# Kernel optimization log

Measured on AMD Instinct MI355X. Metric: run time of the kernel, lower is better.

The kernel has to match this reference:

```python
import jax, jax.numpy as jnp
import numpy as np

REG = 0.05  # reg_param > 0 -> entropic (logsumexp) branch
N, M, D = 16384, 8192, 128


def setup_inputs() -> dict:
    key = jax.random.key(0)
    k1, k2, k3 = jax.random.split(key, 3)
    source_data = jax.random.normal(k1, (N, D), dtype=jnp.float32)
    target_data = jax.random.normal(k2, (M, D), dtype=jnp.float32)
    psi = jax.random.normal(k3, (M,), dtype=jnp.float32) * 0.1
    return {"source_data": source_data, "target_data": target_data, "psi": psi}


def reference(source_data, target_data, psi):
    # squared norms
    ty2 = jnp.sum(target_data ** 2, axis=1)            # [M]
    sx2 = jnp.sum(source_data ** 2, axis=1, keepdims=True)  # [N,1]
    scale = jnp.mean(ty2)                              # scalar normalizer
    # pairwise squared-distance cost, normalized (matches torch expansion)
    cost_xy = (sx2 + ty2[None, :] - 2.0 * source_data @ target_data.T) / scale  # [N,M]
    # entropic semi-dual: -reg * logsumexp((psi - c)/reg) averaged over x
    lse = jax.nn.logsumexp((psi[None, :] - cost_xy) / REG, axis=1)  # [N]
    cte = REG * jnp.log(jnp.asarray(M, dtype=jnp.float32))
    return jnp.mean(-REG * lse) + jnp.mean(psi) + cte
```

## Files before the change

kernel.cpp:

```cpp
#include <hip/hip_runtime.h>
#include <stdint.h>

#define REG_P   0.05f
#define LOG2E   1.4426950408889634f
#define LN2     0.6931471805599453f
#define NSPLIT  8

typedef int   int32x8 __attribute__((ext_vector_type(8)));
typedef float floatx4 __attribute__((ext_vector_type(4)));

__device__ inline int32x8 load32B(const void* p) {
    union { int32x8 v; uint4 q[2]; } u;
    u.q[0] = ((const uint4*)p)[0];
    u.q[1] = ((const uint4*)p)[1];
    return u.v;
}

__device__ inline float block_sum_f(const float* __restrict__ v, int M, int tid,
                                    float* redbuf) {
    float s = 0.f;
    const float4* v4 = (const float4*)v;
    for (int j = tid; j < (M >> 2); j += 256) {
        float4 q = v4[j];
        s += (q.x + q.y) + (q.z + q.w);
    }
    #pragma unroll
    for (int mask = 1; mask < 64; mask <<= 1) s += __shfl_xor(s, mask, 64);
    int wv = tid >> 6, lane = tid & 63;
    if (lane == 0) redbuf[wv] = s;
    __syncthreads();
    return (redbuf[0] + redbuf[1]) + (redbuf[2] + redbuf[3]);
}

__global__ void k1_pack(const float* __restrict__ src, const float* __restrict__ tgt,
                        unsigned char* __restrict__ Sb8, unsigned char* __restrict__ Tbs8,
                        float* __restrict__ sx2, float* __restrict__ ty2,
                        float* __restrict__ out, int N, int M) {
    int tid = threadIdx.x;
    if (blockIdx.x == 0 && tid == 0) out[0] = 0.0f;
    int r16 = tid >> 4;
    int c8  = tid & 15;
    int row_id = blockIdx.x * 16 + r16;
    bool isS = row_id < N;
    int row = isS ? row_id : row_id - N;
    const float4* sp = (const float4*)((isS ? src : tgt) + (size_t)row * 128 + c8 * 8);
    float4 f0 = sp[0], f1 = sp[1];
    int w0 = 0, w1 = 0;
    w0 = __builtin_amdgcn_cvt_pk_fp8_f32(f0.x, f0.y, w0, false);
    w0 = __builtin_amdgcn_cvt_pk_fp8_f32(f0.z, f0.w, w0, true);
    w1 = __builtin_amdgcn_cvt_pk_fp8_f32(f1.x, f1.y, w1, false);
    w1 = __builtin_amdgcn_cvt_pk_fp8_f32(f1.z, f1.w, w1, true);
    uint2 val = make_uint2((unsigned)w0, (unsigned)w1);
    float sq = f0.x*f0.x + f0.y*f0.y + f0.z*f0.z + f0.w*f0.w
             + f1.x*f1.x + f1.y*f1.y + f1.z*f1.z + f1.w*f1.w;
    #pragma unroll
    for (int mask = 1; mask < 16; mask <<= 1) sq += __shfl_xor(sq, mask, 16);
    if (isS) {
        ((uint2*)(Sb8 + (size_t)row * 128 + c8 * 8))[0] = val;
        if (c8 == 0) sx2[row] = sq;
    } else {
        int t = row >> 6, jc = row & 63;
        int ct = jc >> 4, l16 = jc & 15;
        int quad = c8 >> 2, rem = c8 & 3;
        size_t dst = (size_t)t * 8192 + (size_t)((ct * 64 + quad * 16 + l16) * 32 + rem * 8);
        ((uint2*)(Tbs8 + dst))[0] = val;
        if (c8 == 0) ty2[row] = sq;
    }
}

__global__ __launch_bounds__(256, 2) void k3_main(
    const unsigned char* __restrict__ Sb8, const unsigned char* __restrict__ Tbs8,
    const float* __restrict__ psi, const float* __restrict__ ty2,
    float* __restrict__ lpart, int N, int M) {
    __shared__ float sb2a[1024];
    __shared__ float redA[4];
    const int tid  = threadIdx.x;
    const int lane = tid & 63;
    const int wv   = tid >> 6;
    const int quad = lane >> 4, l16 = lane & 15;
    const int b = blockIdx.x;
    const int split = b & 7;
    const int i0 = (b >> 3) * 256;
    const int mspan = M / NSPLIT;
    const int jstart = split * mspan;

    float ty2sum = block_sum_f(ty2, M, tid, redA);
    float scale = ty2sum / (float)M;
    float c1 = 1.0f / (REG_P * scale);
    float a2 = 2.0f * LOG2E / (REG_P * scale);

    for (int idx = tid; idx < mspan; idx += 256) {
        int j = jstart + idx;
        sb2a[idx] = (psi[j] * (1.0f / REG_P) - ty2[j] * c1) * LOG2E;
    }
    __syncthreads();

    int32x8 afrag[4];
    #pragma unroll
    for (int rt = 0; rt < 4; ++rt)
        afrag[rt] = load32B(Sb8 + (size_t)(i0 + wv * 64 + rt * 16 + l16) * 128 + quad * 32);

    float ls[4][4];
    #pragma unroll
    for (int rt = 0; rt < 4; ++rt)
        #pragma unroll
        for (int r = 0; r < 4; ++r) ls[rt][r] = 0.0f;

    const unsigned char* gb = Tbs8 + (size_t)jstart * 128 + (size_t)lane * 32;
    const floatx4 zero4 = (floatx4){0.f, 0.f, 0.f, 0.f};
    const int SC = 0x7F7F7F7F;

    int32x8 bbuf[2][4];
    #pragma unroll
    for (int c = 0; c < 4; ++c) bbuf[0][c] = load32B(gb + c * 2048);

    floatx4 accP[4];
    float bvP = 0.0f;
    bool first = true;

    #pragma unroll 2
    for (int tt = 0; tt < 16; ++tt) {
        const int p = tt & 1;
        if (tt < 15) {
            #pragma unroll
            for (int c = 0; c < 4; ++c)
                bbuf[p ^ 1][c] = load32B(gb + (size_t)((tt + 1) * 4 + c) * 2048);
        }
        #pragma unroll
        for (int c = 0; c < 4; ++c) {
            float bv = sb2a[(tt * 4 + c) * 16 + l16];
            floatx4 a[4];
            #pragma unroll
            for (int rt = 0; rt < 4; ++rt)
                a[rt] = __builtin_amdgcn_mfma_scale_f32_16x16x128_f8f6f4(
                    afrag[rt], bbuf[p][c], zero4, 0, 0, 0, SC, 0, SC);
            if (!first) {
                #pragma unroll
                for (int rt = 0; rt < 4; ++rt)
                    #pragma unroll
                    for (int r = 0; r < 4; ++r)
                        ls[rt][r] += __builtin_amdgcn_exp2f(fmaf(a2, accP[rt][r], bvP));
            }
            #pragma unroll
            for (int rt = 0; rt < 4; ++rt) accP[rt] = a[rt];
            bvP = bv;
            first = false;
        }
    }
    #pragma unroll
    for (int rt = 0; rt < 4; ++rt)
        #pragma unroll
        for (int r = 0; r < 4; ++r)
            ls[rt][r] += __builtin_amdgcn_exp2f(fmaf(a2, accP[rt][r], bvP));

    #pragma unroll
    for (int rt = 0; rt < 4; ++rt)
        #pragma unroll
        for (int r = 0; r < 4; ++r) {
            float v = ls[rt][r];
            #pragma unroll
            for (int mask = 1; mask < 16; mask <<= 1) v += __shfl_xor(v, mask, 64);
            if (l16 == 0) {
                int rowg = i0 + wv * 64 + rt * 16 + quad * 4 + r;
                lpart[(size_t)rowg * NSPLIT + split] = v;
            }
        }
}

__global__ void k4_reduce(const float* __restrict__ lpart,
                          const float* __restrict__ sx2,
                          const float* __restrict__ psi,
                          const float* __restrict__ ty2,
                          float* __restrict__ out, int N, int M) {
    __shared__ float redA[4];
    __shared__ float redB[4];
    int tid = threadIdx.x;
    float ty2s = block_sum_f(ty2, M, tid, redA);
    float scale = ty2s / (float)M;

    int i = blockIdx.x * 256 + tid;
    const float4* lp = (const float4*)(lpart + (size_t)i * NSPLIT);
    float4 p0 = lp[0], p1 = lp[1];
    float s = (p0.x + p0.y + p0.z + p0.w) + (p1.x + p1.y + p1.z + p1.w);
    float L2 = __builtin_amdgcn_logf(s);
    float t = (-REG_P * LN2 * L2 + sx2[i] / scale) * (1.0f / (float)N);
    if (i < M) t += psi[i] * (1.0f / (float)M);
    #pragma unroll
    for (int mask = 1; mask < 64; mask <<= 1) t += __shfl_xor(t, mask, 64);
    int wv = tid >> 6, lane = tid & 63;
    if (lane == 0) redB[wv] = t;
    __syncthreads();
    if (tid == 0) {
        float total = (redB[0] + redB[1]) + (redB[2] + redB[3]);
        if (blockIdx.x == 0) total += REG_P * logf((float)M);
        atomicAdd(out, total);
    }
}

extern "C" void kernel_launch(void* const* d_in, const int* in_sizes, int n_in,
                              void* d_out, int out_size, void* d_ws, size_t ws_size,
                              hipStream_t stream) {
    const float* src = (const float*)d_in[0];
    const float* tgt = (const float*)d_in[1];
    const float* psi = (const float*)d_in[2];
    const int D = 128;
    const int N = in_sizes[0] / D;
    const int M = in_sizes[1] / D;

    char* ws = (char*)d_ws;
    float* sx2   = (float*)ws;
    float* ty2   = (float*)(ws + (size_t)N * 4);
    float* lpart = (float*)(ws + (size_t)N * 4 + (size_t)M * 4);
    size_t off = (size_t)N * 4 + (size_t)M * 4 + (size_t)N * NSPLIT * 4;
    off = (off + 255) & ~(size_t)255;
    unsigned char* Sb8  = (unsigned char*)(ws + off);
    unsigned char* Tbs8 = Sb8 + (size_t)N * 128;

    k1_pack<<<(N + M) / 16, 256, 0, stream>>>(src, tgt, Sb8, Tbs8, sx2, ty2,
                                              (float*)d_out, N, M);
    k3_main<<<(N / 256) * NSPLIT, 256, 0, stream>>>(Sb8, Tbs8, psi, ty2, lpart, N, M);
    k4_reduce<<<N / 256, 256, 0, stream>>>(lpart, sx2, psi, ty2, (float*)d_out, N, M);
}
```

Measured before the change: 100.2 us.

## Halve row tile per block and double occupancy in main MFMA kernel

```diff
diff --git a/kernel.cpp b/kernel.cpp
--- a/kernel.cpp
+++ b/kernel.cpp
@@ -68,7 +68,7 @@
     }
 }
 
-__global__ __launch_bounds__(256, 2) void k3_main(
+__global__ __launch_bounds__(256, 4) void k3_main(
     const unsigned char* __restrict__ Sb8, const unsigned char* __restrict__ Tbs8,
     const float* __restrict__ psi, const float* __restrict__ ty2,
     float* __restrict__ lpart, int N, int M) {
@@ -80,7 +80,7 @@
     const int quad = lane >> 4, l16 = lane & 15;
     const int b = blockIdx.x;
     const int split = b & 7;
-    const int i0 = (b >> 3) * 256;
+    const int i0 = (b >> 3) * 128;
     const int mspan = M / NSPLIT;
     const int jstart = split * mspan;
 
@@ -95,14 +95,14 @@
     }
     __syncthreads();
 
-    int32x8 afrag[4];
-    #pragma unroll
-    for (int rt = 0; rt < 4; ++rt)
-        afrag[rt] = load32B(Sb8 + (size_t)(i0 + wv * 64 + rt * 16 + l16) * 128 + quad * 32);
-
-    float ls[4][4];
-    #pragma unroll
-    for (int rt = 0; rt < 4; ++rt)
+    int32x8 afrag[2];
+    #pragma unroll
+    for (int rt = 0; rt < 2; ++rt)
+        afrag[rt] = load32B(Sb8 + (size_t)(i0 + wv * 32 + rt * 16 + l16) * 128 + quad * 32);
+
+    float ls[2][4];
+    #pragma unroll
+    for (int rt = 0; rt < 2; ++rt)
         #pragma unroll
         for (int r = 0; r < 4; ++r) ls[rt][r] = 0.0f;
 
@@ -110,58 +110,44 @@
     const floatx4 zero4 = (floatx4){0.f, 0.f, 0.f, 0.f};
     const int SC = 0x7F7F7F7F;
 
-    int32x8 bbuf[2][4];
-    #pragma unroll
-    for (int c = 0; c < 4; ++c) bbuf[0][c] = load32B(gb + c * 2048);
-
-    floatx4 accP[4];
+    int32x8 bc = load32B(gb);
+    int32x8 bn = load32B(gb + 2048);
+    floatx4 pA, pB;
     float bvP = 0.0f;
-    bool first = true;
-
-    #pragma unroll 2
-    for (int tt = 0; tt < 16; ++tt) {
-        const int p = tt & 1;
-        if (tt < 15) {
+
+    #pragma unroll 4
+    for (int u = 0; u < 64; ++u) {
+        float bv = sb2a[u * 16 + l16];
+        floatx4 c0 = __builtin_amdgcn_mfma_scale_f32_16x16x128_f8f6f4(
+            afrag[0], bc, zero4, 0, 0, 0, SC, 0, SC);
+        floatx4 c1v = __builtin_amdgcn_mfma_scale_f32_16x16x128_f8f6f4(
+            afrag[1], bc, zero4, 0, 0, 0, SC, 0, SC);
+        int32x8 bf = load32B(gb + (size_t)(u + 2) * 2048);
+        if (u) {
             #pragma unroll
-            for (int c = 0; c < 4; ++c)
-                bbuf[p ^ 1][c] = load32B(gb + (size_t)((tt + 1) * 4 + c) * 2048);
+            for (int r = 0; r < 4; ++r) {
+                ls[0][r] += __builtin_amdgcn_exp2f(fmaf(a2, pA[r], bvP));
+                ls[1][r] += __builtin_amdgcn_exp2f(fmaf(a2, pB[r], bvP));
+            }
         }
-        #pragma unroll
-        for (int c = 0; c < 4; ++c) {
-            float bv = sb2a[(tt * 4 + c) * 16 + l16];
-            floatx4 a[4];
-            #pragma unroll
-            for (int rt = 0; rt < 4; ++rt)
-                a[rt] = __builtin_amdgcn_mfma_scale_f32_16x16x128_f8f6f4(
-                    afrag[rt], bbuf[p][c], zero4, 0, 0, 0, SC, 0, SC);
-            if (!first) {
-                #pragma unroll
-                for (int rt = 0; rt < 4; ++rt)
-                    #pragma unroll
-                    for (int r = 0; r < 4; ++r)
-                        ls[rt][r] += __builtin_amdgcn_exp2f(fmaf(a2, accP[rt][r], bvP));
-            }
-            #pragma unroll
-            for (int rt = 0; rt < 4; ++rt) accP[rt] = a[rt];
-            bvP = bv;
-            first = false;
-        }
-    }
-    #pragma unroll
-    for (int rt = 0; rt < 4; ++rt)
-        #pragma unroll
-        for (int r = 0; r < 4; ++r)
-            ls[rt][r] += __builtin_amdgcn_exp2f(fmaf(a2, accP[rt][r], bvP));
-
-    #pragma unroll
-    for (int rt = 0; rt < 4; ++rt)
+        pA = c0; pB = c1v; bvP = bv;
+        bc = bn; bn = bf;
+    }
+    #pragma unroll
+    for (int r = 0; r < 4; ++r) {
+        ls[0][r] += __builtin_amdgcn_exp2f(fmaf(a2, pA[r], bvP));
+        ls[1][r] += __builtin_amdgcn_exp2f(fmaf(a2, pB[r], bvP));
+    }
+
+    #pragma unroll
+    for (int rt = 0; rt < 2; ++rt)
         #pragma unroll
         for (int r = 0; r < 4; ++r) {
             float v = ls[rt][r];
             #pragma unroll
             for (int mask = 1; mask < 16; mask <<= 1) v += __shfl_xor(v, mask, 64);
             if (l16 == 0) {
-                int rowg = i0 + wv * 64 + rt * 16 + quad * 4 + r;
+                int rowg = i0 + wv * 32 + rt * 16 + quad * 4 + r;
                 lpart[(size_t)rowg * NSPLIT + split] = v;
             }
         }
@@ -218,6 +204,6 @@
 
     k1_pack<<<(N + M) / 16, 256, 0, stream>>>(src, tgt, Sb8, Tbs8, sx2, ty2,
                                               (float*)d_out, N, M);
-    k3_main<<<(N / 256) * NSPLIT, 256, 0, stream>>>(Sb8, Tbs8, psi, ty2, lpart, N, M);
+    k3_main<<<(N / 128) * NSPLIT, 256, 0, stream>>>(Sb8, Tbs8, psi, ty2, lpart, N, M);
     k4_reduce<<<N / 256, 256, 0, stream>>>(lpart, sx2, psi, ty2, (float*)d_out, N, M);
 }
```

Result: faster. 96.33 us (-3.9%).

## Pack source FP8 inside main kernel, fold bias into MFMA accumulator, double split

Applied to the files above, without the earlier changes.

```diff
diff --git a/kernel.cpp b/kernel.cpp
--- a/kernel.cpp
+++ b/kernel.cpp
@@ -4,7 +4,7 @@
 #define REG_P   0.05f
 #define LOG2E   1.4426950408889634f
 #define LN2     0.6931471805599453f
-#define NSPLIT  8
+#define NSPLIT  16
 
 typedef int   int32x8 __attribute__((ext_vector_type(8)));
 typedef float floatx4 __attribute__((ext_vector_type(4)));
@@ -32,18 +32,28 @@
     return (redbuf[0] + redbuf[1]) + (redbuf[2] + redbuf[3]);
 }
 
-__global__ void k1_pack(const float* __restrict__ src, const float* __restrict__ tgt,
-                        unsigned char* __restrict__ Sb8, unsigned char* __restrict__ Tbs8,
-                        float* __restrict__ sx2, float* __restrict__ ty2,
-                        float* __restrict__ out, int N, int M) {
+__device__ inline int32x8 pack_a_frag(const float* __restrict__ p, float a2) {
+    int32x8 out;
+    #pragma unroll
+    for (int i = 0; i < 8; ++i) {
+        float4 f = ((const float4*)p)[i];
+        int w = 0;
+        w = __builtin_amdgcn_cvt_pk_fp8_f32(f.x * a2, f.y * a2, w, false);
+        w = __builtin_amdgcn_cvt_pk_fp8_f32(f.z * a2, f.w * a2, w, true);
+        out[i] = w;
+    }
+    return out;
+}
+
+__global__ void k1_pack(const float* __restrict__ tgt,
+                        unsigned char* __restrict__ Tbs8,
+                        float* __restrict__ ty2, float* __restrict__ out, int M) {
     int tid = threadIdx.x;
     if (blockIdx.x == 0 && tid == 0) out[0] = 0.0f;
     int r16 = tid >> 4;
     int c8  = tid & 15;
-    int row_id = blockIdx.x * 16 + r16;
-    bool isS = row_id < N;
-    int row = isS ? row_id : row_id - N;
-    const float4* sp = (const float4*)((isS ? src : tgt) + (size_t)row * 128 + c8 * 8);
+    int row = blockIdx.x * 16 + r16;
+    const float4* sp = (const float4*)(tgt + (size_t)row * 128 + c8 * 8);
     float4 f0 = sp[0], f1 = sp[1];
     int w0 = 0, w1 = 0;
     w0 = __builtin_amdgcn_cvt_pk_fp8_f32(f0.x, f0.y, w0, false);
@@ -55,32 +65,27 @@
              + f1.x*f1.x + f1.y*f1.y + f1.z*f1.z + f1.w*f1.w;
     #pragma unroll
     for (int mask = 1; mask < 16; mask <<= 1) sq += __shfl_xor(sq, mask, 16);
-    if (isS) {
-        ((uint2*)(Sb8 + (size_t)row * 128 + c8 * 8))[0] = val;
-        if (c8 == 0) sx2[row] = sq;
-    } else {
-        int t = row >> 6, jc = row & 63;
-        int ct = jc >> 4, l16 = jc & 15;
-        int quad = c8 >> 2, rem = c8 & 3;
-        size_t dst = (size_t)t * 8192 + (size_t)((ct * 64 + quad * 16 + l16) * 32 + rem * 8);
-        ((uint2*)(Tbs8 + dst))[0] = val;
-        if (c8 == 0) ty2[row] = sq;
-    }
-}
-
-__global__ __launch_bounds__(256, 2) void k3_main(
-    const unsigned char* __restrict__ Sb8, const unsigned char* __restrict__ Tbs8,
+    int t = row >> 6, jc = row & 63;
+    int ct = jc >> 4, l16 = jc & 15;
+    int quad = c8 >> 2, rem = c8 & 3;
+    size_t dst = (size_t)t * 8192 + (size_t)((ct * 64 + quad * 16 + l16) * 32 + rem * 8);
+    ((uint2*)(Tbs8 + dst))[0] = val;
+    if (c8 == 0) ty2[row] = sq;
+}
+
+__global__ __launch_bounds__(256, 4) void k3_main(
+    const float* __restrict__ src, const unsigned char* __restrict__ Tbs8,
     const float* __restrict__ psi, const float* __restrict__ ty2,
     float* __restrict__ lpart, int N, int M) {
-    __shared__ float sb2a[1024];
+    __shared__ float sb2a[512];
     __shared__ float redA[4];
     const int tid  = threadIdx.x;
     const int lane = tid & 63;
     const int wv   = tid >> 6;
     const int quad = lane >> 4, l16 = lane & 15;
     const int b = blockIdx.x;
-    const int split = b & 7;
-    const int i0 = (b >> 3) * 256;
+    const int split = b & 15;
+    const int i0 = (b >> 4) * 256;
     const int mspan = M / NSPLIT;
     const int jstart = split * mspan;
 
@@ -98,7 +103,8 @@
     int32x8 afrag[4];
     #pragma unroll
     for (int rt = 0; rt < 4; ++rt)
-        afrag[rt] = load32B(Sb8 + (size_t)(i0 + wv * 64 + rt * 16 + l16) * 128 + quad * 32);
+        afrag[rt] = pack_a_frag(
+            src + (size_t)(i0 + wv * 64 + rt * 16 + l16) * 128 + quad * 32, a2);
 
     float ls[4][4];
     #pragma unroll
@@ -107,51 +113,40 @@
         for (int r = 0; r < 4; ++r) ls[rt][r] = 0.0f;
 
     const unsigned char* gb = Tbs8 + (size_t)jstart * 128 + (size_t)lane * 32;
-    const floatx4 zero4 = (floatx4){0.f, 0.f, 0.f, 0.f};
     const int SC = 0x7F7F7F7F;
 
-    int32x8 bbuf[2][4];
-    #pragma unroll
-    for (int c = 0; c < 4; ++c) bbuf[0][c] = load32B(gb + c * 2048);
-
+    int32x8 bc = load32B(gb);
+    int32x8 bn = load32B(gb + 2048);
     floatx4 accP[4];
-    float bvP = 0.0f;
     bool first = true;
 
-    #pragma unroll 2
-    for (int tt = 0; tt < 16; ++tt) {
-        const int p = tt & 1;
-        if (tt < 15) {
-            #pragma unroll
-            for (int c = 0; c < 4; ++c)
-                bbuf[p ^ 1][c] = load32B(gb + (size_t)((tt + 1) * 4 + c) * 2048);
-        }
-        #pragma unroll
-        for (int c = 0; c < 4; ++c) {
-            float bv = sb2a[(tt * 4 + c) * 16 + l16];
-            floatx4 a[4];
+    #pragma unroll 4
+    for (int u = 0; u < 32; ++u) {
+        float bv = sb2a[u * 16 + l16];
+        floatx4 bv4 = (floatx4){bv, bv, bv, bv};
+        floatx4 a[4];
+        #pragma unroll
+        for (int rt = 0; rt < 4; ++rt)
+            a[rt] = __builtin_amdgcn_mfma_scale_f32_16x16x128_f8f6f4(
+                afrag[rt], bc, bv4, 0, 0, 0, SC, 0, SC);
+        int32x8 bf = load32B(gb + (size_t)(u + 2) * 2048);
+        if (!first) {
             #pragma unroll
             for (int rt = 0; rt < 4; ++rt)
-                a[rt] = __builtin_amdgcn_mfma_scale_f32_16x16x128_f8f6f4(
-                    afrag[rt], bbuf[p][c], zero4, 0, 0, 0, SC, 0, SC);
-            if (!first) {
                 #pragma unroll
-                for (int rt = 0; rt < 4; ++rt)
-                    #pragma unroll
-                    for (int r = 0; r < 4; ++r)
-                        ls[rt][r] += __builtin_amdgcn_exp2f(fmaf(a2, accP[rt][r], bvP));
-            }
-            #pragma unroll
-            for (int rt = 0; rt < 4; ++rt) accP[rt] = a[rt];
-            bvP = bv;
-            first = false;
+                for (int r = 0; r < 4; ++r)
+                    ls[rt][r] += __builtin_amdgcn_exp2f(accP[rt][r]);
         }
+        #pragma unroll
+        for (int rt = 0; rt < 4; ++rt) accP[rt] = a[rt];
+        bc = bn; bn = bf;
+        first = false;
     }
     #pragma unroll
     for (int rt = 0; rt < 4; ++rt)
         #pragma unroll
         for (int r = 0; r < 4; ++r)
-            ls[rt][r] += __builtin_amdgcn_exp2f(fmaf(a2, accP[rt][r], bvP));
+            ls[rt][r] += __builtin_amdgcn_exp2f(accP[rt][r]);
 
     #pragma unroll
     for (int rt = 0; rt < 4; ++rt)
@@ -168,7 +163,7 @@
 }
 
 __global__ void k4_reduce(const float* __restrict__ lpart,
-                          const float* __restrict__ sx2,
+                          const float* __restrict__ src,
                           const float* __restrict__ psi,
                           const float* __restrict__ ty2,
                           float* __restrict__ out, int N, int M) {
@@ -180,11 +175,28 @@
 
     int i = blockIdx.x * 256 + tid;
     const float4* lp = (const float4*)(lpart + (size_t)i * NSPLIT);
-    float4 p0 = lp[0], p1 = lp[1];
-    float s = (p0.x + p0.y + p0.z + p0.w) + (p1.x + p1.y + p1.z + p1.w);
+    float s = 0.f;
+    #pragma unroll
+    for (int q = 0; q < NSPLIT / 4; ++q) {
+        float4 p = lp[q];
+        s += (p.x + p.y) + (p.z + p.w);
+    }
     float L2 = __builtin_amdgcn_logf(s);
-    float t = (-REG_P * LN2 * L2 + sx2[i] / scale) * (1.0f / (float)N);
+    float t = -REG_P * LN2 * L2 * (1.0f / (float)N);
     if (i < M) t += psi[i] * (1.0f / (float)M);
+
+    {
+        const float4* s4 = (const float4*)src;
+        int per_block = (N * 128 / 4) / gridDim.x;
+        int base = blockIdx.x * per_block;
+        float s2 = 0.f;
+        for (int j = base + tid; j < base + per_block; j += 256) {
+            float4 q = s4[j];
+            s2 += (q.x*q.x + q.y*q.y) + (q.z*q.z + q.w*q.w);
+        }
+        t += s2 / ((float)N * scale);
+    }
+
     #pragma unroll
     for (int mask = 1; mask < 64; mask <<= 1) t += __shfl_xor(t, mask, 64);
     int wv = tid >> 6, lane = tid & 63;
@@ -208,16 +220,13 @@
     const int M = in_sizes[1] / D;
 
     char* ws = (char*)d_ws;
-    float* sx2   = (float*)ws;
-    float* ty2   = (float*)(ws + (size_t)N * 4);
-    float* lpart = (float*)(ws + (size_t)N * 4 + (size_t)M * 4);
-    size_t off = (size_t)N * 4 + (size_t)M * 4 + (size_t)N * NSPLIT * 4;
+    float* ty2   = (float*)ws;
+    float* lpart = (float*)(ws + (size_t)M * 4);
+    size_t off = (size_t)M * 4 + (size_t)N * NSPLIT * 4;
     off = (off + 255) & ~(size_t)255;
-    unsigned char* Sb8  = (unsigned char*)(ws + off);
-    unsigned char* Tbs8 = Sb8 + (size_t)N * 128;
-
-    k1_pack<<<(N + M) / 16, 256, 0, stream>>>(src, tgt, Sb8, Tbs8, sx2, ty2,
-                                              (float*)d_out, N, M);
-    k3_main<<<(N / 256) * NSPLIT, 256, 0, stream>>>(Sb8, Tbs8, psi, ty2, lpart, N, M);
-    k4_reduce<<<N / 256, 256, 0, stream>>>(lpart, sx2, psi, ty2, (float*)d_out, N, M);
-}
+    unsigned char* Tbs8 = (unsigned char*)(ws + off);
+
+    k1_pack<<<M / 16, 256, 0, stream>>>(tgt, Tbs8, ty2, (float*)d_out, M);
+    k3_main<<<(N / 256) * NSPLIT, 256, 0, stream>>>(src, Tbs8, psi, ty2, lpart, N, M);
+    k4_reduce<<<N / 256, 256, 0, stream>>>(lpart, src, psi, ty2, (float*)d_out, N, M);
+}
```

Measured after the change: 116.6 us. 16.3% more time.
